# Kernel tuning notes

Hardware: AMD Instinct MI355X
Metric: run time of the kernel (lower is better)

Reference implementation:

```python
import jax, jax.numpy as jnp
import numpy as np

EPS = 1e-5

def conv2d(x, w, b=None, pad=0):
    y = jax.lax.conv_general_dilated(x, w, (1, 1), [(pad, pad), (pad, pad)],
                                     dimension_numbers=('NCHW', 'OIHW', 'NCHW'))
    if b is not None:
        y = y + b[None, :, None, None]
    return y

def bn(x, w, b, m, v):
    scale = w / jnp.sqrt(v + EPS)
    return x * scale[None, :, None, None] + (b - m * scale)[None, :, None, None]

def setup_inputs() -> dict:
    key = jax.random.key(0)
    ks = jax.random.split(key, 24)
    B, Cin, H, W = 4, 2048, 60, 60
    Ci = Cin // 4           # inter_channels = 512
    Cq = Ci // 8            # q/k dim = 64
    Cout = 59
    r = lambda k, s, sc=0.05: jax.random.normal(k, s, jnp.float32) * sc
    return {
        'x': jax.random.normal(ks[0], (B, Cin, H, W), jnp.float32),
        'dep': jax.random.uniform(ks[1], (B, 1, H, W), jnp.float32),
        'w5a': r(ks[2], (Ci, Cin, 3, 3)),
        'bn1_w': jax.random.uniform(ks[3], (Ci,), jnp.float32, 0.5, 1.5),
        'bn1_b': r(ks[4], (Ci,)),
        'bn1_m': r(ks[5], (Ci,)),
        'bn1_v': jax.random.uniform(ks[6], (Ci,), jnp.float32, 0.5, 1.5),
        'wq': r(ks[7], (Cq, Ci, 1, 1)), 'bq': r(ks[8], (Cq,)),
        'wk': r(ks[9], (Cq, Ci, 1, 1)), 'bk': r(ks[10], (Cq,)),
        'wv': r(ks[11], (Ci, Ci, 1, 1)), 'bv': r(ks[12], (Ci,)),
        'gamma': r(ks[13], (1,), 0.5),
        'lamb1': r(ks[14], (1,), 0.5),
        'w51': r(ks[15], (Ci, Ci, 3, 3)),
        'bn2_w': jax.random.uniform(ks[16], (Ci,), jnp.float32, 0.5, 1.5),
        'bn2_b': r(ks[17], (Ci,)),
        'bn2_m': r(ks[18], (Ci,)),
        'bn2_v': jax.random.uniform(ks[19], (Ci,), jnp.float32, 0.5, 1.5),
        'w6': r(ks[20], (Cout, Ci, 1, 1)), 'b6': r(ks[21], (Cout,)),
    }

def reference(x, dep, w5a, bn1_w, bn1_b, bn1_m, bn1_v, wq, bq, wk, bk, wv, bv,
              gamma, lamb1, w51, bn2_w, bn2_b, bn2_m, bn2_v, w6, b6):
    # conv5a: 3x3 conv -> BN (inference) -> ReLU
    f1 = jax.nn.relu(bn(conv2d(x, w5a, pad=1), bn1_w, bn1_b, bn1_m, bn1_v))
    B, C, H, W = f1.shape
    N = H * W
    q = conv2d(f1, wq, bq).reshape(B, -1, N)     # [B, C/8, N]
    k = conv2d(f1, wk, bk).reshape(B, -1, N)     # [B, C/8, N]
    v = conv2d(f1, wv, bv).reshape(B, C, N)      # [B, C, N]
    energy = jnp.einsum('bci,bcj->bij', q, k)    # [B, N, N]
    d1 = dep.reshape(B, 1, N)
    d = jnp.transpose(d1, (0, 2, 1)) - d1        # [B, N, N] depth difference
    sim = energy - lamb1[0] * jnp.square(d)      # dep_order == 2
    attn = jax.nn.softmax(sim, axis=-1)
    # out[b,c,i] = sum_j v[b,c,j] * attn[b,i,j]  (bmm with attn^T)
    out = jnp.einsum('bcj,bij->bci', v, attn).reshape(B, C, H, W)
    sa = gamma[0] * out + f1
    sc = jax.nn.relu(bn(conv2d(sa, w51, pad=1), bn2_w, bn2_b, bn2_m, bn2_v))
    # Dropout2d in eval mode is identity
    logits = conv2d(sc, w6, b6)
    return (logits,)
```

## Files before the change

kernel.cpp:

```cpp
#include <hip/hip_runtime.h>
#include <math.h>

typedef unsigned short u16;
typedef short s16x8 __attribute__((ext_vector_type(8)));
typedef float f32x4 __attribute__((ext_vector_type(4)));

#define HW 3600
#define WID 60
#define SIMS 3616
#define AROWS 3712
#define SP 4216
#define PCIN 2048

__device__ __forceinline__ u16 f2bf(float f){
  unsigned u = __float_as_uint(f);
  unsigned r = (u + 0x7fffu + ((u>>16)&1u)) >> 16;
  return (u16)r;
}
__device__ __forceinline__ float bf2f(u16 b){ return __uint_as_float(((unsigned)b)<<16); }

__device__ __forceinline__ void gl2lds16(const void* g, void* l){
  __builtin_amdgcn_global_load_lds((const __attribute__((address_space(1))) unsigned*)g,
                                   (__attribute__((address_space(3))) unsigned*)l, 16, 0, 0);
}

__device__ __forceinline__ float4 ldg4(const float* __restrict__ p){
  return *reinterpret_cast<const float4*>(p);
}

__global__ void bn_prep(const float* __restrict__ w1, const float* __restrict__ b1,
                        const float* __restrict__ m1, const float* __restrict__ v1,
                        const float* __restrict__ w2, const float* __restrict__ b2,
                        const float* __restrict__ m2, const float* __restrict__ v2,
                        float* __restrict__ sc1, float* __restrict__ sh1,
                        float* __restrict__ sc2, float* __restrict__ sh2){
  int i = threadIdx.x;
  if(i < 512){
    float s1 = w1[i] / sqrtf(v1[i] + 1e-5f);
    sc1[i] = s1; sh1[i] = b1[i] - m1[i]*s1;
    float s2 = w2[i] / sqrtf(v2[i] + 1e-5f);
    sc2[i] = s2; sh2[i] = b2[i] - m2[i]*s2;
  }
}

__global__ __launch_bounds__(256) void pack_x(const float* __restrict__ x, u16* __restrict__ xpadT){
  __shared__ float tile[64][65];
  const int b = blockIdx.z, sp0 = blockIdx.x*64, ci0 = blockIdx.y*64;
  const int t = threadIdx.x, tc = t & 63, tr = t >> 6;
  const float* xb = x + ((size_t)b*PCIN + ci0)*HW;
  #pragma unroll
  for(int l=0;l<16;l++){
    int ci = tr + l*4;
    int sp = sp0 + tc;
    float v = 0.f;
    if(sp < SP){
      int j = sp / 68, c = sp - j*68;
      int jj = j-1, cc = c-1;
      if((unsigned)jj < 60u && (unsigned)cc < 60u) v = xb[(size_t)ci*HW + jj*60 + cc];
    }
    tile[ci][tc] = v;
  }
  __syncthreads();
  const size_t PL = (size_t)4*SP*PCIN;
  u16* outb = xpadT + (size_t)b*SP*PCIN;
  #pragma unroll
  for(int l=0;l<16;l++){
    int spr = tr + l*4;
    int sp = sp0 + spr;
    if(sp < SP){
      float v = tile[tc][spr];
      u16 hh = f2bf(v);
      u16 ll = f2bf(v - bf2f(hh));
      size_t o = (size_t)sp*PCIN + ci0 + tc;
      outb[o] = hh;
      outb[o + PL] = ll;
    }
  }
}

__global__ __launch_bounds__(256) void pack_w5a(const float* __restrict__ w, u16* __restrict__ out){
  const int ci = blockIdx.x*256 + threadIdx.x;
  const int m  = blockIdx.y;
  const int rs = blockIdx.z;
  float v = w[((size_t)m*PCIN + ci)*9 + rs];
  u16 hh = f2bf(v);
  u16 ll = f2bf(v - bf2f(hh));
  size_t base = ((size_t)rs*512 + m)*6144;
  out[base + ci]        = hh;
  out[base + 2048 + ci] = ll;
  out[base + 4096 + ci] = hh;
}

__global__ __launch_bounds__(256) void pack_w51(const float* __restrict__ w, u16* __restrict__ out){
  const int ci = blockIdx.x*256 + threadIdx.x;
  const int m  = blockIdx.y;
  const int rs = blockIdx.z;
  float v = w[((size_t)m*512 + ci)*9 + rs];
  out[((size_t)rs*512 + m)*512 + ci] = f2bf(v);
}

template<int MODE>
__global__ __launch_bounds__(256) void mfma_gemm(
    const u16* __restrict__ A, const u16* __restrict__ B,
    const float* __restrict__ scale, const float* __restrict__ shift,
    const float* __restrict__ f1, const float* __restrict__ gamma,
    float* __restrict__ outF, u16* __restrict__ outH)
{
  constexpr int CIC = (MODE==0)? 2048 : 512;
  constexpr int KRS = (MODE==0)? 6144 : 512;
  constexpr int KPR = KRS/32;
  constexpr int NSTEP = (MODE==2)? (SIMS/32) : (9*KPR);
  constexpr int NB  = (MODE==2)? 29 : 30;
  constexpr int GCHUNK = (16*NB) >> 3;

  __shared__ __align__(16) u16 lds[3*8192];

  const int t  = threadIdx.x;

  const int wg = blockIdx.x;
  const int wgid = (wg & 7)*GCHUNK + (wg >> 3);
  const int mt = wgid / (4*NB);
  const int nt = wgid - mt*(4*NB);
  const int m0 = mt << 7;
  const int b  = nt / NB;
  const int nb = nt - b*NB;

  const int rowA = ((t>>6)<<4) + (t&15);
  const int chnk = (t>>4)&3;

  const u16* Ap[2]; const u16* Bp[2];
  #pragma unroll
  for(int p=0;p<2;p++){
    int r = rowA + p*64;
    if constexpr(MODE==2) Ap[p] = A + (size_t)b*512*SIMS + (size_t)(m0+r)*SIMS + chnk*8;
    else                  Ap[p] = A + (size_t)(m0+r)*KRS + chnk*8;
    if constexpr(MODE==2){
      Bp[p] = B + (size_t)b*AROWS*SIMS + (size_t)(nb*128 + r)*SIMS + chnk*8;
    } else {
      int spb = (nb*2 + p)*68 + rowA;
      Bp[p] = B + (size_t)b*SP*CIC + (size_t)spb*CIC + chnk*8;
    }
  }
  const size_t PL = (size_t)4*SP*PCIN;

  f32x4 acc[4][4];
  #pragma unroll
  for(int i=0;i<4;i++)
    #pragma unroll
    for(int j=0;j<4;j++) acc[i][j] = (f32x4){0.f,0.f,0.f,0.f};

  const int lane = t & 63;
  const int wv = t >> 6;
  const int wm = (wv >> 1) << 6;
  const int wn = (wv & 1) << 6;
  const int fr = lane & 15, fq = lane >> 4;
  const char* ldsc = (const char*)lds;
  const int abase = (wm >> 4)*1024 + fq*256 + fr*16;
  const int bbase = 8192 + (wn >> 4)*1024 + fq*256 + fr*16;

  auto stage = [&](int st, int q){
    int rs = 0, k0;
    if constexpr(MODE==2){ k0 = st << 5; }
    else { rs = st / KPR; k0 = (st - rs*KPR) << 5; }
    size_t aoffg; size_t boffg;
    int plane = 0, ci0 = 0, rsh = 0;
    if constexpr(MODE==2){ aoffg = k0; boffg = k0; }
    else {
      aoffg = (size_t)rs*512*KRS + k0;
      int r3 = rs/3, s3 = rs - r3*3;
      plane = (MODE==0)? (k0 >> 12) : 0;
      ci0 = k0 & (CIC-1);
      boffg = (size_t)plane*PL + (size_t)(r3*68 + s3)*CIC + ci0;
    }
    u16* lb = &lds[q*8192];
    #pragma unroll
    for(int p=0;p<2;p++){
      gl2lds16(Ap[p] + aoffg, lb + p*2048 + t*8);
      gl2lds16(Bp[p] + boffg, lb + 4096 + p*2048 + t*8);
    }
  };

  auto compute = [&](int q){
    const char* base = ldsc + q*16384;
    s16x8 af[4], bg[4];
    #pragma unroll
    for(int i=0;i<4;i++) af[i] = *(const s16x8*)(base + abase + i*1024);
    #pragma unroll
    for(int j=0;j<4;j++) bg[j] = *(const s16x8*)(base + bbase + j*1024);
    __builtin_amdgcn_s_setprio(1);
    #pragma unroll
    for(int i=0;i<4;i++)
      #pragma unroll
      for(int j=0;j<4;j++)
        acc[i][j] = __builtin_amdgcn_mfma_f32_16x16x32_bf16(af[i], bg[j], acc[i][j], 0,0,0);
    __builtin_amdgcn_s_setprio(0);
  };

  stage(0, 0);
  stage(1, 1);
  int cur = 0;
  for(int st = 0; st < NSTEP-2; ++st){
    int q2 = cur + 2; if(q2 >= 3) q2 -= 3;
    stage(st+2, q2);
    asm volatile("s_waitcnt vmcnt(8)" ::: "memory");
    __builtin_amdgcn_s_barrier();
    asm volatile("" ::: "memory");
    compute(cur);
    asm volatile("" ::: "memory");
    __builtin_amdgcn_s_barrier();
    asm volatile("" ::: "memory");
    cur = (cur+1 == 3)? 0 : cur+1;
  }
  asm volatile("s_waitcnt vmcnt(4)" ::: "memory");
  __builtin_amdgcn_s_barrier();
  asm volatile("" ::: "memory");
  compute(cur);
  cur = (cur+1 == 3)? 0 : cur+1;
  asm volatile("s_waitcnt vmcnt(0)" ::: "memory");
  __builtin_amdgcn_s_barrier();
  asm volatile("" ::: "memory");
  compute(cur);

  if constexpr(MODE==0 || MODE==1){
    #pragma unroll
    for(int i=0;i<4;i++){
      #pragma unroll
      for(int q=0;q<4;q++){
        int m = m0 + wm + i*16 + fq*4 + q;
        float scl = scale[m], shf = shift[m];
        #pragma unroll
        for(int j=0;j<4;j++){
          int np = nb*128 + wn + j*16 + fr;
          int h = np>>6, w = np&63;
          if(w < 60){
            float v = fmaxf(fmaf(acc[i][j][q], scl, shf), 0.f);
            size_t o = ((size_t)b*512 + m)*HW + h*60 + w;
            if constexpr(MODE==0) outF[o] = v;
            else                  outH[o] = f2bf(v);
          }
        }
      }
    }
  } else {
    float g = gamma[0];
    #pragma unroll
    for(int j=0;j<4;j++){
      int ip = nb*128 + wn + j*16 + fr;
      if(ip < HW){
        int h = ip/60, w = ip - h*60;
        size_t spo = (size_t)b*SP*512 + (size_t)((h+1)*68 + (w+1))*512;
        #pragma unroll
        for(int i=0;i<4;i++){
          #pragma unroll
          for(int q=0;q<4;q++){
            int m = m0 + wm + i*16 + fq*4 + q;
            float v = fmaf(g, acc[i][j][q], f1[((size_t)b*512 + m)*HW + ip]);
            outH[spo + m] = f2bf(v);
          }
        }
      }
    }
  }
}

template<bool INBF, bool GM, bool OUTBF>
__global__ __launch_bounds__(256) void gemm1x1(const void* __restrict__ inv,
    const float* __restrict__ w, const float* __restrict__ bias,
    float* __restrict__ outF, u16* __restrict__ outH, int M, int K, int OS)
{
  const int b  = blockIdx.z;
  const int m0 = blockIdx.x * 64;
  const int n0 = blockIdx.y * 64;
  const int t  = threadIdx.x;
  const int tm = t >> 4, tn = t & 15;

  __shared__ __align__(16) float As[16][64];
  __shared__ __align__(16) float Bs[16][64];

  float acc[4][4] = {};

  const int arow = t >> 2, acol = (t & 3) << 2;
  const int bkk  = t & 15, bnl  = (t >> 4) << 2;
  const bool bvalid = (n0 + bnl) < HW;

  for(int k0 = 0; k0 < K; k0 += 16){
    float4 av = make_float4(0.f,0.f,0.f,0.f);
    if(!GM || (m0 + arow) < M)
      av = ldg4(&w[(size_t)(m0 + arow)*K + k0 + acol]);
    As[acol+0][arow] = av.x;
    As[acol+1][arow] = av.y;
    As[acol+2][arow] = av.z;
    As[acol+3][arow] = av.w;

    float4 bv = make_float4(0.f,0.f,0.f,0.f);
    if(bvalid){
      if constexpr(INBF){
        const u16* inb = (const u16*)inv + (size_t)b*K*HW;
        const u16* p = &inb[(size_t)(k0 + bkk)*HW + n0 + bnl];
        bv.x = bf2f(p[0]); bv.y = bf2f(p[1]); bv.z = bf2f(p[2]); bv.w = bf2f(p[3]);
      } else {
        const float* inb = (const float*)inv + (size_t)b*K*HW;
        bv = ldg4(&inb[(size_t)(k0 + bkk)*HW + n0 + bnl]);
      }
    }
    *reinterpret_cast<float4*>(&Bs[bkk][bnl]) = bv;

    __syncthreads();
    #pragma unroll
    for(int kk=0;kk<16;kk++){
      float4 a  = *reinterpret_cast<const float4*>(&As[kk][tm<<2]);
      float4 bb = *reinterpret_cast<const float4*>(&Bs[kk][tn<<2]);
      float ar[4] = {a.x,a.y,a.z,a.w};
      float br[4] = {bb.x,bb.y,bb.z,bb.w};
      #pragma unroll
      for(int ii=0;ii<4;ii++)
        #pragma unroll
        for(int jj=0;jj<4;jj++)
          acc[ii][jj] = fmaf(ar[ii], br[jj], acc[ii][jj]);
    }
    __syncthreads();
  }

  int n = n0 + (tn<<2);
  if(n < OS){
    #pragma unroll
    for(int ii=0;ii<4;ii++){
      int m = m0 + (tm<<2) + ii;
      if(!GM || m < M){
        float bi = bias[m];
        #pragma unroll
        for(int jj=0;jj<4;jj++){
          int nn = n + jj;
          float val = (nn < HW) ? (acc[ii][jj] + bi) : 0.f;
          if constexpr(OUTBF) outH[((size_t)b*M + m)*OS + nn] = f2bf(val);
          else                outF[((size_t)b*M + m)*OS + nn] = val;
        }
      }
    }
  }
}

__global__ __launch_bounds__(256) void energy_sim(
    const float* __restrict__ q, const float* __restrict__ kptr,
    const float* __restrict__ dep, const float* __restrict__ lamb1,
    float* __restrict__ sim)
{
  const int i0 = blockIdx.y * 64;
  const int j0 = blockIdx.x * 64;
  const int t  = threadIdx.x;
  const int tm = t >> 4, tn = t & 15;

  __shared__ __align__(16) float Qs[64][64];
  __shared__ __align__(16) float Ks[64][64];

  {
    const int cc = t >> 4;
    const int il = (t & 15) << 2;
    #pragma unroll
    for(int it=0; it<4; it++){
      int c = cc + it*16;
      float4 qv = make_float4(0.f,0.f,0.f,0.f);
      float4 kv = make_float4(0.f,0.f,0.f,0.f);
      if(i0 + il < HW) qv = ldg4(&q[(size_t)c*HW + i0 + il]);
      if(j0 + il < HW) kv = ldg4(&kptr[(size_t)c*HW + j0 + il]);
      *reinterpret_cast<float4*>(&Qs[c][il]) = qv;
      *reinterpret_cast<float4*>(&Ks[c][il]) = kv;
    }
  }
  __syncthreads();

  float acc[4][4] = {};
  #pragma unroll 4
  for(int c=0;c<64;c++){
    float4 a  = *reinterpret_cast<const float4*>(&Qs[c][tm<<2]);
    float4 bv = *reinterpret_cast<const float4*>(&Ks[c][tn<<2]);
    float ar[4] = {a.x,a.y,a.z,a.w};
    float br[4] = {bv.x,bv.y,bv.z,bv.w};
    #pragma unroll
    for(int ii=0;ii<4;ii++)
      #pragma unroll
      for(int jj=0;jj<4;jj++)
        acc[ii][jj] = fmaf(ar[ii], br[jj], acc[ii][jj]);
  }

  float lam = lamb1[0];
  float di[4], dj[4];
  #pragma unroll
  for(int ii=0;ii<4;ii++){ int i = i0+(tm<<2)+ii; di[ii] = (i<HW)? dep[i] : 0.f; }
  #pragma unroll
  for(int jj=0;jj<4;jj++){ int j = j0+(tn<<2)+jj; dj[jj] = (j<HW)? dep[j] : 0.f; }

  int j = j0 + (tn<<2);
  if(j < HW){
    #pragma unroll
    for(int ii=0;ii<4;ii++){
      int i = i0 + (tm<<2) + ii;
      if(i < HW){
        float4 o;
        float d0 = di[ii]-dj[0]; o.x = acc[ii][0] - lam*d0*d0;
        float d1 = di[ii]-dj[1]; o.y = acc[ii][1] - lam*d1*d1;
        float d2 = di[ii]-dj[2]; o.z = acc[ii][2] - lam*d2*d2;
        float d3 = di[ii]-dj[3]; o.w = acc[ii][3] - lam*d3*d3;
        *reinterpret_cast<float4*>(&sim[(size_t)i*SIMS + j]) = o;
      }
    }
  }
}

__global__ __launch_bounds__(256) void softmax_attn(const float* __restrict__ sim,
                                                    u16* __restrict__ attn){
  __shared__ float redM[4], redS[4];
  const int row = blockIdx.x;
  const float* p = sim + (size_t)row*SIMS;
  u16*   a = attn + (size_t)row*SIMS;
  const int wid = threadIdx.x >> 6, lane = threadIdx.x & 63;

  float m = -3.4e38f, s = 0.f;
  for(int j=threadIdx.x; j<HW; j+=256){
    float v = p[j];
    float mo = m;
    m = fmaxf(m, v);
    s = s*__expf(mo - m) + __expf(v - m);
  }
  #pragma unroll
  for(int o=32;o>0;o>>=1){
    float m2 = __shfl_xor(m, o, 64);
    float s2 = __shfl_xor(s, o, 64);
    float mn = fmaxf(m, m2);
    s = s*__expf(m - mn) + s2*__expf(m2 - mn);
    m = mn;
  }
  if(lane==0){ redM[wid] = m; redS[wid] = s; }
  __syncthreads();
  float M = fmaxf(fmaxf(redM[0],redM[1]), fmaxf(redM[2],redM[3]));
  float S = redS[0]*__expf(redM[0]-M) + redS[1]*__expf(redM[1]-M)
          + redS[2]*__expf(redM[2]-M) + redS[3]*__expf(redM[3]-M);
  float inv = 1.0f / S;
  for(int j=threadIdx.x; j<HW; j+=256) a[j] = f2bf(__expf(p[j]-M) * inv);
  if(threadIdx.x < SIMS-HW) a[HW + threadIdx.x] = 0;
}

extern "C" void kernel_launch(void* const* d_in, const int* in_sizes, int n_in,
                              void* d_out, int out_size, void* d_ws, size_t ws_size,
                              hipStream_t stream)
{
  const float* x    = (const float*)d_in[0];
  const float* dep  = (const float*)d_in[1];
  const float* w5a  = (const float*)d_in[2];
  const float* bn1w = (const float*)d_in[3];
  const float* bn1b = (const float*)d_in[4];
  const float* bn1m = (const float*)d_in[5];
  const float* bn1v = (const float*)d_in[6];
  const float* wq   = (const float*)d_in[7];
  const float* bq   = (const float*)d_in[8];
  const float* wk   = (const float*)d_in[9];
  const float* bk   = (const float*)d_in[10];
  const float* wv   = (const float*)d_in[11];
  const float* bv   = (const float*)d_in[12];
  const float* gamma= (const float*)d_in[13];
  const float* lamb1= (const float*)d_in[14];
  const float* w51  = (const float*)d_in[15];
  const float* bn2w = (const float*)d_in[16];
  const float* bn2b = (const float*)d_in[17];
  const float* bn2m = (const float*)d_in[18];
  const float* bn2v = (const float*)d_in[19];
  const float* w6   = (const float*)d_in[20];
  const float* b6   = (const float*)d_in[21];
  float* out = (float*)d_out;

  char* cur = (char*)d_ws;
  auto alloc = [&](size_t bytes)->char*{ char* p = cur; cur += (bytes + 255) & ~(size_t)255; return p; };

  float* sc1 = (float*)alloc(512*4);
  float* sh1 = (float*)alloc(512*4);
  float* sc2 = (float*)alloc(512*4);
  float* sh2 = (float*)alloc(512*4);
  u16* xpadT = (u16*)alloc((size_t)2*4*SP*PCIN*2);
  u16* W5ab  = (u16*)alloc((size_t)9*512*6144*2);
  u16* W51b  = (u16*)alloc((size_t)9*512*512*2);
  float* f1  = (float*)alloc((size_t)4*512*HW*4);
  float* qb  = (float*)alloc((size_t)4*64*HW*4);
  float* kb  = (float*)alloc((size_t)4*64*HW*4);
  u16* vb    = (u16*)alloc((size_t)4*512*SIMS*2);
  float* sim = (float*)alloc((size_t)HW*SIMS*4);
  u16* attn  = (u16*)alloc((size_t)4*AROWS*SIMS*2);
  u16* sapadT= (u16*)alloc((size_t)4*SP*512*2);
  u16* scb   = (u16*)alloc((size_t)4*512*HW*2);

  bn_prep<<<1, 512, 0, stream>>>(bn1w,bn1b,bn1m,bn1v, bn2w,bn2b,bn2m,bn2v,
                                 sc1,sh1,sc2,sh2);

  hipMemsetAsync(sapadT, 0, (size_t)4*SP*512*2, stream);

  pack_x  <<<dim3(66,32,4), 256, 0, stream>>>(x, xpadT);
  pack_w5a<<<dim3(8,512,9), 256, 0, stream>>>(w5a, W5ab);
  pack_w51<<<dim3(2,512,9), 256, 0, stream>>>(w51, W51b);

  mfma_gemm<0><<<480, 256, 0, stream>>>(W5ab, xpadT, sc1, sh1,
                                        nullptr, nullptr, f1, nullptr);

  gemm1x1<false,false,false><<<dim3(1,57,4), 256, 0, stream>>>(f1, wq, bq, qb, nullptr, 64, 512, HW);
  gemm1x1<false,false,false><<<dim3(1,57,4), 256, 0, stream>>>(f1, wk, bk, kb, nullptr, 64, 512, HW);
  gemm1x1<false,false,true ><<<dim3(8,57,4), 256, 0, stream>>>(f1, wv, bv, nullptr, vb, 512, 512, SIMS);

  for(int b=0;b<4;b++){
    energy_sim<<<dim3(57,57), 256, 0, stream>>>(qb + (size_t)b*64*HW,
                                                kb + (size_t)b*64*HW,
                                                dep + (size_t)b*HW, lamb1, sim);
    softmax_attn<<<HW, 256, 0, stream>>>(sim, attn + (size_t)b*AROWS*SIMS);
  }

  mfma_gemm<2><<<464, 256, 0, stream>>>(vb, attn, nullptr, nullptr,
                                        f1, gamma, nullptr, sapadT);

  mfma_gemm<1><<<480, 256, 0, stream>>>(W51b, sapadT, sc2, sh2,
                                        nullptr, nullptr, nullptr, scb);

  gemm1x1<true,true,false><<<dim3(1,57,4), 256, 0, stream>>>(scb, w6, b6, out, nullptr, 59, 512, HW);
}
```

Baseline: 2.642 ms.

## Split conv5a GEMM K dimension three ways and reduce partials in separate kernel

The 3x3 conv5a implicit GEMM is split along the filter-tap dimension into three groups, tripling the grid from 480 to 1440 workgroups so more CUs are busy. Each group writes raw fp32 partial sums into the reused sim buffer, and a new reduce kernel sums the three partials and applies BN scale/shift and ReLU to produce f1. This adds extra global traffic for the partial buffers and one extra launch in exchange for better occupancy on the large K loop.

```diff
diff --git a/kernel.cpp b/kernel.cpp
--- a/kernel.cpp
+++ b/kernel.cpp
@@ -109,9 +109,12 @@
   constexpr int CIC = (MODE==0)? 2048 : 512;
   constexpr int KRS = (MODE==0)? 6144 : 512;
   constexpr int KPR = KRS/32;
-  constexpr int NSTEP = (MODE==2)? (SIMS/32) : (9*KPR);
+  constexpr int GS  = (MODE==0)? 3 : 1;
+  constexpr int NSTEP = (MODE==2)? (SIMS/32) : ((9/GS)*KPR);
   constexpr int NB  = (MODE==2)? 29 : 30;
-  constexpr int GCHUNK = (16*NB) >> 3;
+  constexpr int NT  = 4*NB;
+  constexpr int PERG = 4*NT;
+  constexpr int GCHUNK = (GS*PERG) >> 3;
 
   __shared__ __align__(16) u16 lds[3*8192];
 
@@ -119,8 +122,10 @@
 
   const int wg = blockIdx.x;
   const int wgid = (wg & 7)*GCHUNK + (wg >> 3);
-  const int mt = wgid / (4*NB);
-  const int nt = wgid - mt*(4*NB);
+  const int g  = wgid / PERG;
+  const int rr = wgid - g*PERG;
+  const int mt = rr / NT;
+  const int nt = rr - mt*NT;
   const int m0 = mt << 7;
   const int b  = nt / NB;
   const int nb = nt - b*NB;
@@ -161,15 +166,14 @@
   auto stage = [&](int st, int q){
     int rs = 0, k0;
     if constexpr(MODE==2){ k0 = st << 5; }
-    else { rs = st / KPR; k0 = (st - rs*KPR) << 5; }
+    else { int sq = st / KPR; rs = g*(9/GS) + sq; k0 = (st - sq*KPR) << 5; }
     size_t aoffg; size_t boffg;
-    int plane = 0, ci0 = 0, rsh = 0;
     if constexpr(MODE==2){ aoffg = k0; boffg = k0; }
     else {
       aoffg = (size_t)rs*512*KRS + k0;
       int r3 = rs/3, s3 = rs - r3*3;
-      plane = (MODE==0)? (k0 >> 12) : 0;
-      ci0 = k0 & (CIC-1);
+      int plane = (MODE==0)? (k0 >> 12) : 0;
+      int ci0 = k0 & (CIC-1);
       boffg = (size_t)plane*PL + (size_t)(r3*68 + s3)*CIC + ci0;
     }
     u16* lb = &lds[q*8192];
@@ -221,7 +225,24 @@
   asm volatile("" ::: "memory");
   compute(cur);
 
-  if constexpr(MODE==0 || MODE==1){
+  if constexpr(MODE==0){
+    float* po = outF + (size_t)g*4*512*HW;
+    #pragma unroll
+    for(int i=0;i<4;i++){
+      #pragma unroll
+      for(int q=0;q<4;q++){
+        int m = m0 + wm + i*16 + fq*4 + q;
+        #pragma unroll
+        for(int j=0;j<4;j++){
+          int np = nb*128 + wn + j*16 + fr;
+          int h = np>>6, w = np&63;
+          if(w < 60){
+            po[((size_t)b*512 + m)*HW + h*60 + w] = acc[i][j][q];
+          }
+        }
+      }
+    }
+  } else if constexpr(MODE==1){
     #pragma unroll
     for(int i=0;i<4;i++){
       #pragma unroll
@@ -234,15 +255,13 @@
           int h = np>>6, w = np&63;
           if(w < 60){
             float v = fmaxf(fmaf(acc[i][j][q], scl, shf), 0.f);
-            size_t o = ((size_t)b*512 + m)*HW + h*60 + w;
-            if constexpr(MODE==0) outF[o] = v;
-            else                  outH[o] = f2bf(v);
+            outH[((size_t)b*512 + m)*HW + h*60 + w] = f2bf(v);
           }
         }
       }
     }
   } else {
-    float g = gamma[0];
+    float g2 = gamma[0];
     #pragma unroll
     for(int j=0;j<4;j++){
       int ip = nb*128 + wn + j*16 + fr;
@@ -254,13 +273,33 @@
           #pragma unroll
           for(int q=0;q<4;q++){
             int m = m0 + wm + i*16 + fq*4 + q;
-            float v = fmaf(g, acc[i][j][q], f1[((size_t)b*512 + m)*HW + ip]);
+            float v = fmaf(g2, acc[i][j][q], f1[((size_t)b*512 + m)*HW + ip]);
             outH[spo + m] = f2bf(v);
           }
         }
       }
     }
   }
+}
+
+__global__ __launch_bounds__(256) void reduce_f1(const float* __restrict__ p,
+                                                 const float* __restrict__ scale,
+                                                 const float* __restrict__ shift,
+                                                 float* __restrict__ f1){
+  const size_t P4 = (size_t)4*512*HW/4;
+  size_t i = (size_t)blockIdx.x*256 + threadIdx.x;
+  if(i >= P4) return;
+  float4 a = ldg4((const float*)p + i*4);
+  float4 b = ldg4((const float*)p + (P4+i)*4);
+  float4 c = ldg4((const float*)p + (2*P4+i)*4);
+  int m = (int)((i*4/HW) & 511);
+  float scl = scale[m], shf = shift[m];
+  float4 o;
+  o.x = fmaxf(fmaf(a.x+b.x+c.x, scl, shf), 0.f);
+  o.y = fmaxf(fmaf(a.y+b.y+c.y, scl, shf), 0.f);
+  o.z = fmaxf(fmaf(a.z+b.z+c.z, scl, shf), 0.f);
+  o.w = fmaxf(fmaf(a.w+b.w+c.w, scl, shf), 0.f);
+  *reinterpret_cast<float4*>(&f1[i*4]) = o;
 }
 
 template<bool INBF, bool GM, bool OUTBF>
@@ -487,6 +526,8 @@
   u16* sapadT= (u16*)alloc((size_t)4*SP*512*2);
   u16* scb   = (u16*)alloc((size_t)4*512*HW*2);
 
+  float* part = sim;
+
   bn_prep<<<1, 512, 0, stream>>>(bn1w,bn1b,bn1m,bn1v, bn2w,bn2b,bn2m,bn2v,
                                  sc1,sh1,sc2,sh2);
 
@@ -496,8 +537,9 @@
   pack_w5a<<<dim3(8,512,9), 256, 0, stream>>>(w5a, W5ab);
   pack_w51<<<dim3(2,512,9), 256, 0, stream>>>(w51, W51b);
 
-  mfma_gemm<0><<<480, 256, 0, stream>>>(W5ab, xpadT, sc1, sh1,
-                                        nullptr, nullptr, f1, nullptr);
+  mfma_gemm<0><<<1440, 256, 0, stream>>>(W5ab, xpadT, nullptr, nullptr,
+                                         nullptr, nullptr, part, nullptr);
+  reduce_f1<<<(4*512*HW/4 + 255)/256, 256, 0, stream>>>(part, sc1, sh1, f1);
 
   gemm1x1<false,false,false><<<dim3(1,57,4), 256, 0, stream>>>(f1, wq, bq, qb, nullptr, 64, 512, HW);
   gemm1x1<false,false,false><<<dim3(1,57,4), 256, 0, stream>>>(f1, wk, bk, kb, nullptr, 64, 512, HW);
```

After: 2.661 ms. About the same (+0.7%).
